# Kernel tuning notes

Measured on AMD Instinct MI355X. Metric: run time of the kernel, lower is better.

The kernel has to match this reference:

```python
import jax, jax.numpy as jnp
import numpy as np
from jax import lax


def _conv2d(x, w, b, pad):
    out = lax.conv_general_dilated(x, w, window_strides=(1, 1),
                                   padding=[(pad, pad), (pad, pad)])
    return out + b[None, :, None, None]


def _modulated_deform_conv(x, off_w, off_b, w, b, k, pad):
    """Modulated deformable conv (deformable_groups=1, stride=1, 'same' pad)."""
    B, C, H, W = x.shape
    K2 = k * k
    # offset/mask conv: 3*K2 channels -> (dy, dx, mask_logits)
    om = _conv2d(x, off_w, off_b, pad)              # [B, 3*K2, H, W]
    dy, dx, mlog = om[:, :K2], om[:, K2:2 * K2], om[:, 2 * K2:]
    mask = jax.nn.sigmoid(mlog)                     # [B, K2, H, W]

    xp = jnp.pad(x, ((0, 0), (0, 0), (pad, pad), (pad, pad)))
    Hp, Wp = H + 2 * pad, W + 2 * pad
    Ho, Wo = H, W                                   # stride 1, pad = k//2

    ky, kx = jnp.meshgrid(jnp.arange(k), jnp.arange(k), indexing='ij')
    ky = ky.reshape(1, K2, 1, 1).astype(x.dtype)
    kx = kx.reshape(1, K2, 1, 1).astype(x.dtype)
    iy = jnp.arange(Ho, dtype=x.dtype).reshape(1, 1, Ho, 1)
    ix = jnp.arange(Wo, dtype=x.dtype).reshape(1, 1, 1, Wo)

    py = iy + ky + dy                               # [B, K2, Ho, Wo] sample y (padded coords)
    px = ix + kx + dx                               # [B, K2, Ho, Wo] sample x

    y0f = jnp.floor(py); x0f = jnp.floor(px)
    ty = py - y0f; tx = px - x0f
    y0 = y0f.astype(jnp.int32); x0 = x0f.astype(jnp.int32)
    y1 = y0 + 1; x1 = x0 + 1

    xp_flat = xp.reshape(B, C, Hp * Wp)

    def gather(yi, xi):
        valid = ((yi >= 0) & (yi < Hp) & (xi >= 0) & (xi < Wp)).astype(x.dtype)
        yc = jnp.clip(yi, 0, Hp - 1)
        xc = jnp.clip(xi, 0, Wp - 1)
        idx = (yc * Wp + xc).reshape(B, 1, K2 * Ho * Wo)
        v = jnp.take_along_axis(xp_flat, idx, axis=2).reshape(B, C, K2, Ho, Wo)
        return v * valid[:, None]                   # zero-pad outside

    w00 = ((1 - ty) * (1 - tx))[:, None]
    w01 = ((1 - ty) * tx)[:, None]
    w10 = (ty * (1 - tx))[:, None]
    w11 = (ty * tx)[:, None]

    cols = (gather(y0, x0) * w00 + gather(y0, x1) * w01 +
            gather(y1, x0) * w10 + gather(y1, x1) * w11)
    cols = cols * mask[:, None]                     # [B, C, K2, Ho, Wo]

    O = w.shape[0]
    out = jnp.einsum('bckhw,ock->bohw', cols, w.reshape(O, C, K2))
    return out + b[None, :, None, None]


def setup_inputs() -> dict:
    key = jax.random.key(0)
    ks = jax.random.split(key, 12)
    B, Cin, H, W = 8, 64, 56, 56
    Ch = 128  # out_channels // 2

    def rn(k, shape, scale):
        return jax.random.normal(k, shape, dtype=jnp.float32) * scale

    return {
        'x': rn(ks[0], (B, Cin, H, W), 1.0),
        'w3': rn(ks[1], (Ch, Cin, 3, 3), 0.05),
        'b3': rn(ks[2], (Ch,), 0.05),
        'off3_w': rn(ks[3], (3 * 9, Cin, 3, 3), 0.01),
        'off3_b': rn(ks[4], (3 * 9,), 0.01),
        'w5': rn(ks[5], (Ch, Cin, 5, 5), 0.03),
        'b5': rn(ks[6], (Ch,), 0.05),
        'off5_w': rn(ks[7], (3 * 25, Cin, 5, 5), 0.01),
        'off5_b': rn(ks[8], (3 * 25,), 0.01),
        'sub_w': rn(ks[9], (Ch, Cin, 1, 1), 0.1),
        'sub_b': rn(ks[10], (Ch,), 0.05),
    }


def reference(x, w3, b3, off3_w, off3_b, w5, b5, off5_w, off5_b, sub_w, sub_b):
    x3 = _modulated_deform_conv(x, off3_w, off3_b, w3, b3, k=3, pad=1)
    x5 = _modulated_deform_conv(x, off5_w, off5_b, w5, b5, k=5, pad=2)
    xs = _conv2d(x, sub_w, sub_b, pad=0)            # 1x1 shortcut projection
    x3 = x3 + xs
    x5 = x5 + xs
    out = jnp.concatenate((x3, x5), axis=1)
    return jax.nn.relu(out)
```

## Files before the change

### kernel.cpp

```cpp
#include <hip/hip_runtime.h>
#include <math.h>

typedef __attribute__((ext_vector_type(8))) short short8;
typedef __attribute__((ext_vector_type(4))) float f32x4;

#define US_XP    0
#define N_XP     (8*60*60*64)
#define US_WOFF  (US_XP + N_XP)
#define N_WOFF   (25*2*8*64*8)
#define US_W5    (US_WOFF + N_WOFF)
#define N_W5     (26*2*8*64*8)
#define US_W3    (US_W5 + N_W5)
#define N_W3     (10*2*8*64*8)
#define US_TOT   (US_W3 + N_W3)
#define FB_BYTES (((US_TOT*2) + 15) & ~15)
#define F_BOM    0
#define F_B5     128
#define F_B3     256
#define F_OM     384
#define N_OM     (8*128*3136)

__device__ __forceinline__ unsigned short f2bf(float f) {
    union { float f; unsigned u; } v; v.f = f;
    unsigned r = v.u + 0x7FFFu + ((v.u >> 16) & 1u);
    return (unsigned short)(r >> 16);
}
__device__ __forceinline__ float bf2f(unsigned short u) {
    union { unsigned u; float f; } v; v.u = ((unsigned)u) << 16; return v.f;
}

__global__ __launch_bounds__(256) void prep_kernel(
    const float* __restrict__ x,
    const float* __restrict__ w3, const float* __restrict__ b3,
    const float* __restrict__ off3w, const float* __restrict__ off3b,
    const float* __restrict__ w5, const float* __restrict__ b5,
    const float* __restrict__ off5w, const float* __restrict__ off5b,
    const float* __restrict__ subw, const float* __restrict__ subb,
    unsigned short* __restrict__ us, float* __restrict__ fb)
{
    const int NTOT = US_TOT + 384;
    for (int i = blockIdx.x*256 + threadIdx.x; i < NTOT; i += gridDim.x*256) {
        if (i < US_TOT) {
            float v = 0.f;
            if (i < US_WOFF) {
                int c = i & 63, t = i >> 6;
                int xx = t % 60; t /= 60;
                int yy = t % 60; int b = t / 60;
                int y = yy - 2, xc = xx - 2;
                if ((unsigned)y < 56u && (unsigned)xc < 56u)
                    v = x[((b*64 + c)*56 + y)*56 + xc];
            } else {
                int j, mode;
                if (i < US_W5)      { j = i - US_WOFF; mode = 0; }
                else if (i < US_W3) { j = i - US_W5;   mode = 1; }
                else                { j = i - US_W3;   mode = 2; }
                int j8   = j & 7;
                int lane = (j >> 3) & 63;
                int oct  = (j >> 9) & 7;
                int kt   = (j >> 12) & 1;
                int tap  = j >> 13;
                int oc   = oct*16 + (lane & 15);
                int c    = kt*32 + (lane >> 4)*8 + j8;
                if (mode == 0) {
                    if (oc < 27) {
                        int ky = tap/5, kx = tap%5;
                        if (ky>=1 && ky<=3 && kx>=1 && kx<=3)
                            v = off3w[((oc*64 + c)*3 + (ky-1))*3 + (kx-1)];
                    } else if (oc < 102) {
                        v = off5w[((oc-27)*64 + c)*25 + tap];
                    }
                } else if (mode == 1) {
                    v = (tap < 25) ? w5[(oc*64 + c)*25 + tap] : subw[oc*64 + c];
                } else {
                    v = (tap < 9) ? w3[(oc*64 + c)*9 + tap] : subw[oc*64 + c];
                }
            }
            us[i] = f2bf(v);
        } else {
            int fj = i - US_TOT;
            float v;
            if (fj < 128)      v = (fj < 27) ? off3b[fj] : ((fj < 102) ? off5b[fj-27] : 0.f);
            else if (fj < 256) { int o = fj-128; v = b5[o] + subb[o]; }
            else               { int o = fj-256; v = b3[o] + subb[o]; }
            fb[fj] = v;
        }
    }
}

template<bool DEFORM>
__global__ __launch_bounds__(256, 3) void convm(
    const unsigned short* __restrict__ xp,
    const float* __restrict__ om,
    float* __restrict__ out,
    const unsigned short* __restrict__ wpA, const float* __restrict__ biasA,
    const unsigned short* __restrict__ wpB, const float* __restrict__ biasB,
    int ksA, int ksB, int ntA, int ntB, int omc0A, int omc0B,
    int outc0A, int outc0B, int out_cs)
{
    const int z = blockIdx.z;
    const unsigned short* wp = z ? wpB : wpA;
    const float* bias = z ? biasB : biasA;
    const int KS    = z ? ksB : ksA;
    const int ntaps = z ? ntB : ntA;
    const int omc0  = z ? omc0B : omc0A;
    const int outc0 = z ? outc0B : outc0A;
    const int K2 = KS*KS;
    const int PAD = (KS == 3) ? 1 : 2;
    const int SHIFT = 2 - PAD;
    const int HP = 56 + 2*PAD;

    const int b    = blockIdx.y;
    const int pix0 = blockIdx.x * 32;
    const int lane = threadIdx.x & 63;
    const int wave = threadIdx.x >> 6;
    const int r15  = lane & 15;
    const int q4   = lane >> 4;

    __shared__ unsigned short cols[2][32*72];

    f32x4 acc[2][2] = {{{0.f,0.f,0.f,0.f},{0.f,0.f,0.f,0.f}},
                       {{0.f,0.f,0.f,0.f},{0.f,0.f,0.f,0.f}}};

    const unsigned short* xpb = xp + (size_t)b * (60*60*64);

    auto stage = [&](int tap, unsigned short* buf) {
        const int cl = r15 * 4;
        int ky = 0, kx = 0;
        if (tap < K2) { ky = tap / KS; kx = tap - ky*KS; }
#pragma unroll
        for (int it = 0; it < 2; ++it) {
            const int px  = wave*8 + it*4 + q4;
            const int pix = pix0 + px;
            const int oy  = pix / 56;
            const int ox  = pix - oy*56;
            ushort4 val;
            if (DEFORM && tap < K2) {
                const float dy = om[(size_t)(b*128 + omc0 + tap)*3136 + pix];
                const float dx = om[(size_t)(b*128 + omc0 + K2 + tap)*3136 + pix];
                const float ml = om[(size_t)(b*128 + omc0 + 2*K2 + tap)*3136 + pix];
                const float mask = 1.f / (1.f + __expf(-ml));
                const float py = (float)(oy + ky) + dy;
                const float qx = (float)(ox + kx) + dx;
                const float y0f = floorf(py), x0f = floorf(qx);
                const float ty = py - y0f, tx = qx - x0f;
                const int y0 = (int)y0f, x0 = (int)x0f;
                const int y1 = y0 + 1,   x1 = x0 + 1;
                float w00 = (1.f-ty)*(1.f-tx)*mask;
                float w01 = (1.f-ty)*tx*mask;
                float w10 = ty*(1.f-tx)*mask;
                float w11 = ty*tx*mask;
                const bool vy0 = (y0>=0)&(y0<HP), vy1 = (y1>=0)&(y1<HP);
                const bool vx0 = (x0>=0)&(x0<HP), vx1 = (x1>=0)&(x1<HP);
                if (!(vy0&vx0)) w00 = 0.f;
                if (!(vy0&vx1)) w01 = 0.f;
                if (!(vy1&vx0)) w10 = 0.f;
                if (!(vy1&vx1)) w11 = 0.f;
                const int yc0 = min(max(y0,0),HP-1)+SHIFT;
                const int yc1 = min(max(y1,0),HP-1)+SHIFT;
                const int xc0 = min(max(x0,0),HP-1)+SHIFT;
                const int xc1 = min(max(x1,0),HP-1)+SHIFT;
                ushort4 u00 = *(const ushort4*)(xpb + (yc0*60+xc0)*64 + cl);
                ushort4 u01 = *(const ushort4*)(xpb + (yc0*60+xc1)*64 + cl);
                ushort4 u10 = *(const ushort4*)(xpb + (yc1*60+xc0)*64 + cl);
                ushort4 u11 = *(const ushort4*)(xpb + (yc1*60+xc1)*64 + cl);
                val.x = f2bf(bf2f(u00.x)*w00 + bf2f(u01.x)*w01 + bf2f(u10.x)*w10 + bf2f(u11.x)*w11);
                val.y = f2bf(bf2f(u00.y)*w00 + bf2f(u01.y)*w01 + bf2f(u10.y)*w10 + bf2f(u11.y)*w11);
                val.z = f2bf(bf2f(u00.z)*w00 + bf2f(u01.z)*w01 + bf2f(u10.z)*w10 + bf2f(u11.z)*w11);
                val.w = f2bf(bf2f(u00.w)*w00 + bf2f(u01.w)*w01 + bf2f(u10.w)*w10 + bf2f(u11.w)*w11);
            } else {
                int yy, xx;
                if (DEFORM) { yy = oy + 2; xx = ox + 2; }
                else        { yy = oy + ky + SHIFT; xx = ox + kx + SHIFT; }
                val = *(const ushort4*)(xpb + (yy*60+xx)*64 + cl);
            }
            *(ushort4*)&buf[px*72 + cl] = val;
        }
    };

    auto gemm = [&](int tap, const unsigned short* buf) {
#pragma unroll
        for (int kt = 0; kt < 2; ++kt) {
            const unsigned short* wt = wp + ((size_t)((tap*2 + kt)*8 + wave*2)*64 + lane)*8;
            short8 a0 = *(const short8*)wt;
            short8 a1 = *(const short8*)(wt + 64*8);
            const unsigned short* bp = buf + r15*72 + kt*32 + q4*8;
            short8 b0 = *(const short8*)bp;
            short8 b1 = *(const short8*)(bp + 16*72);
            acc[0][0] = __builtin_amdgcn_mfma_f32_16x16x32_bf16(a0, b0, acc[0][0], 0, 0, 0);
            acc[1][0] = __builtin_amdgcn_mfma_f32_16x16x32_bf16(a1, b0, acc[1][0], 0, 0, 0);
            acc[0][1] = __builtin_amdgcn_mfma_f32_16x16x32_bf16(a0, b1, acc[0][1], 0, 0, 0);
            acc[1][1] = __builtin_amdgcn_mfma_f32_16x16x32_bf16(a1, b1, acc[1][1], 0, 0, 0);
        }
    };

    stage(0, cols[0]);
    __syncthreads();
    for (int t = 0; t < ntaps; ++t) {
        if (t + 1 < ntaps) stage(t + 1, cols[(t+1) & 1]);
        gemm(t, cols[t & 1]);
        __syncthreads();
    }

#pragma unroll
    for (int j = 0; j < 2; ++j) {
#pragma unroll
        for (int pt = 0; pt < 2; ++pt) {
#pragma unroll
            for (int reg = 0; reg < 4; ++reg) {
                const int oc  = (wave*2 + j)*16 + q4*4 + reg;
                const int pix = pix0 + pt*16 + r15;
                float v = acc[j][pt][reg] + bias[oc];
                if (DEFORM) v = fmaxf(v, 0.f);
                out[((size_t)b*out_cs + outc0 + oc)*3136 + pix] = v;
            }
        }
    }
}

extern "C" void kernel_launch(void* const* d_in, const int* in_sizes, int n_in,
                              void* d_out, int out_size, void* d_ws, size_t ws_size,
                              hipStream_t stream)
{
    (void)in_sizes; (void)n_in; (void)out_size; (void)ws_size;
    const float* x     = (const float*)d_in[0];
    const float* w3    = (const float*)d_in[1];
    const float* b3    = (const float*)d_in[2];
    const float* off3w = (const float*)d_in[3];
    const float* off3b = (const float*)d_in[4];
    const float* w5    = (const float*)d_in[5];
    const float* b5    = (const float*)d_in[6];
    const float* off5w = (const float*)d_in[7];
    const float* off5b = (const float*)d_in[8];
    const float* subw  = (const float*)d_in[9];
    const float* subb  = (const float*)d_in[10];

    unsigned short* us = (unsigned short*)d_ws;
    float* fb  = (float*)((char*)d_ws + FB_BYTES);
    float* omb = fb + F_OM;
    float* out = (float*)d_out;

    prep_kernel<<<dim3(1024), dim3(256), 0, stream>>>(
        x, w3, b3, off3w, off3b, w5, b5, off5w, off5b, subw, subb, us, fb);

    convm<false><<<dim3(98, 8, 1), dim3(256), 0, stream>>>(
        us + US_XP, nullptr, omb,
        us + US_WOFF, fb + F_BOM, us + US_WOFF, fb + F_BOM,
        5, 5, 25, 25, 0, 0, 0, 0, 128);

    convm<true><<<dim3(98, 8, 2), dim3(256), 0, stream>>>(
        us + US_XP, omb, out,
        us + US_W5, fb + F_B5, us + US_W3, fb + F_B3,
        5, 3, 26, 10, 27, 0, 128, 0, 256);
}
```

Baseline: 187.0 us.

## Precompute deform sampling offsets/weights and widen gathers with larger pixel tiles

A new meta kernel precomputes, for every tap and pixel, the four bilinear corner byte offsets and bf16-packed mask-scaled weights, so the deformable conv no longer computes the sigmoid, floor and clamps inline. The staging loop now loads 16-byte channel chunks (8 lanes per pixel) rather than 8-byte ones. It blends with packed bf16 conversions. The deformable conv uses 64-pixel tiles, with the 3x3/5x5 branch interleaved on blockIdx.x instead of z. The trade-off is an extra launch plus writing and re-reading the offset/weight buffers, and bf16 rounding of the interpolation weights.

New measurement: 190.9 us. 2.1% more time.

```diff
diff --git a/kernel.cpp b/kernel.cpp
--- a/kernel.cpp
+++ b/kernel.cpp
@@ -1,4 +1,5 @@
 #include <hip/hip_runtime.h>
+#include <hip/hip_bf16.h>
 #include <math.h>
 
 typedef __attribute__((ext_vector_type(8))) short short8;
@@ -19,14 +20,26 @@
 #define F_B3     256
 #define F_OM     384
 #define N_OM     (8*128*3136)
+#define N_ITEMS  (8*34*3136)
+#define F_OFFS   (F_OM + N_OM)
+#define F_WTS    (F_OFFS + N_ITEMS*4)
 
 __device__ __forceinline__ unsigned short f2bf(float f) {
     union { float f; unsigned u; } v; v.f = f;
     unsigned r = v.u + 0x7FFFu + ((v.u >> 16) & 1u);
     return (unsigned short)(r >> 16);
 }
-__device__ __forceinline__ float bf2f(unsigned short u) {
-    union { unsigned u; float f; } v; v.u = ((unsigned)u) << 16; return v.f;
+__device__ __forceinline__ unsigned pack2(float lo, float hi) {
+    __hip_bfloat162 h = __float22bfloat162_rn(make_float2(lo, hi));
+    return *(unsigned*)&h;
+}
+__device__ __forceinline__ unsigned blend2(unsigned a, unsigned b, unsigned c, unsigned d,
+                                           float w00, float w01, float w10, float w11) {
+    float lo = __uint_as_float(a << 16) * w00 + __uint_as_float(b << 16) * w01
+             + __uint_as_float(c << 16) * w10 + __uint_as_float(d << 16) * w11;
+    float hi = __uint_as_float(a & 0xffff0000u) * w00 + __uint_as_float(b & 0xffff0000u) * w01
+             + __uint_as_float(c & 0xffff0000u) * w10 + __uint_as_float(d & 0xffff0000u) * w11;
+    return pack2(lo, hi);
 }
 
 __global__ __launch_bounds__(256) void prep_kernel(
@@ -87,109 +100,140 @@
     }
 }
 
-template<bool DEFORM>
+__global__ __launch_bounds__(256) void meta_kernel(
+    const float* __restrict__ om, int4* __restrict__ offs, uint2* __restrict__ wts)
+{
+    const int idx = blockIdx.x*256 + threadIdx.x;
+    const int pix = idx % 3136;
+    const int r   = idx / 3136;
+    const int t   = r % 34;
+    const int b   = r / 34;
+    int ky, kx, cdy, cdx, cml, HP, SH;
+    if (t < 25) { ky = t/5;  kx = t%5;  cdy = 27+t; cdx = 52+t; cml = 77+t; HP = 60; SH = 0; }
+    else { int tt = t-25; ky = tt/3; kx = tt%3; cdy = tt; cdx = 9+tt; cml = 18+tt; HP = 58; SH = 1; }
+    const int oy = pix/56, ox = pix - oy*56;
+    const size_t base = (size_t)b*128*3136 + pix;
+    const float dy = om[base + (size_t)cdy*3136];
+    const float dx = om[base + (size_t)cdx*3136];
+    const float ml = om[base + (size_t)cml*3136];
+    const float mask = 1.f / (1.f + __expf(-ml));
+    const float py = (float)(oy + ky) + dy;
+    const float qx = (float)(ox + kx) + dx;
+    const float y0f = floorf(py), x0f = floorf(qx);
+    const float ty = py - y0f, tx = qx - x0f;
+    const int y0 = (int)y0f, x0 = (int)x0f, y1 = y0+1, x1 = x0+1;
+    float w00 = (1.f-ty)*(1.f-tx)*mask;
+    float w01 = (1.f-ty)*tx*mask;
+    float w10 = ty*(1.f-tx)*mask;
+    float w11 = ty*tx*mask;
+    const bool vy0 = (unsigned)y0 < (unsigned)HP, vy1 = (unsigned)y1 < (unsigned)HP;
+    const bool vx0 = (unsigned)x0 < (unsigned)HP, vx1 = (unsigned)x1 < (unsigned)HP;
+    if (!(vy0 && vx0)) w00 = 0.f;
+    if (!(vy0 && vx1)) w01 = 0.f;
+    if (!(vy1 && vx0)) w10 = 0.f;
+    if (!(vy1 && vx1)) w11 = 0.f;
+    const int yc0 = min(max(y0,0),HP-1)+SH, yc1 = min(max(y1,0),HP-1)+SH;
+    const int xc0 = min(max(x0,0),HP-1)+SH, xc1 = min(max(x1,0),HP-1)+SH;
+    offs[idx] = make_int4((yc0*60+xc0)<<7, (yc0*60+xc1)<<7, (yc1*60+xc0)<<7, (yc1*60+xc1)<<7);
+    wts[idx]  = make_uint2(pack2(w00,w01), pack2(w10,w11));
+}
+
+template<int PXT, bool DEFORM>
 __global__ __launch_bounds__(256, 3) void convm(
     const unsigned short* __restrict__ xp,
-    const float* __restrict__ om,
+    const int4* __restrict__ offs, const uint2* __restrict__ wts,
     float* __restrict__ out,
     const unsigned short* __restrict__ wpA, const float* __restrict__ biasA,
     const unsigned short* __restrict__ wpB, const float* __restrict__ biasB,
-    int ksA, int ksB, int ntA, int ntB, int omc0A, int omc0B,
+    int ntA, int ntB, int k2A, int k2B, int tofsA, int tofsB,
     int outc0A, int outc0B, int out_cs)
 {
-    const int z = blockIdx.z;
-    const unsigned short* wp = z ? wpB : wpA;
-    const float* bias = z ? biasB : biasA;
-    const int KS    = z ? ksB : ksA;
-    const int ntaps = z ? ntB : ntA;
-    const int omc0  = z ? omc0B : omc0A;
-    const int outc0 = z ? outc0B : outc0A;
-    const int K2 = KS*KS;
-    const int PAD = (KS == 3) ? 1 : 2;
-    const int SHIFT = 2 - PAD;
-    const int HP = 56 + 2*PAD;
+    const int kind  = DEFORM ? (int)(blockIdx.x & 1) : 0;
+    const int pxblk = DEFORM ? (int)(blockIdx.x >> 1) : (int)blockIdx.x;
+    const unsigned short* wp = kind ? wpB : wpA;
+    const float* bias = kind ? biasB : biasA;
+    const int ntaps = kind ? ntB : ntA;
+    const int K2    = kind ? k2B : k2A;
+    const int tofs  = kind ? tofsB : tofsA;
+    const int outc0 = kind ? outc0B : outc0A;
 
     const int b    = blockIdx.y;
-    const int pix0 = blockIdx.x * 32;
+    const int pix0 = pxblk * PXT;
     const int lane = threadIdx.x & 63;
     const int wave = threadIdx.x >> 6;
-    const int r15  = lane & 15;
-    const int q4   = lane >> 4;
-
-    __shared__ unsigned short cols[2][32*72];
-
-    f32x4 acc[2][2] = {{{0.f,0.f,0.f,0.f},{0.f,0.f,0.f,0.f}},
-                       {{0.f,0.f,0.f,0.f},{0.f,0.f,0.f,0.f}}};
-
-    const unsigned short* xpb = xp + (size_t)b * (60*60*64);
+    const int r15 = lane & 15, q4 = lane >> 4;
+    const int cg  = lane & 7,  pr = lane >> 3;
+
+    constexpr int NIT = PXT / 32;
+    constexpr int NPT = PXT / 16;
+
+    __shared__ unsigned short cols[2][PXT*72];
+
+    f32x4 acc[2][NPT];
+#pragma unroll
+    for (int i = 0; i < 2; ++i)
+#pragma unroll
+        for (int pt = 0; pt < NPT; ++pt) acc[i][pt] = (f32x4){0.f,0.f,0.f,0.f};
+
+    const unsigned short* xpb = xp + (size_t)b*(60*60*64);
+    const char* xb = (const char*)xpb;
+
+    int coff[NIT], mbase[NIT];
+#pragma unroll
+    for (int it = 0; it < NIT; ++it) {
+        const int px  = wave*(NIT*8) + it*8 + pr;
+        const int pix = pix0 + px;
+        const int oy  = pix/56, ox = pix - oy*56;
+        coff[it]  = (((oy+2)*60) + ox + 2) << 7;
+        mbase[it] = (b*34 + tofs)*3136 + pix;
+    }
 
     auto stage = [&](int tap, unsigned short* buf) {
-        const int cl = r15 * 4;
-        int ky = 0, kx = 0;
-        if (tap < K2) { ky = tap / KS; kx = tap - ky*KS; }
-#pragma unroll
-        for (int it = 0; it < 2; ++it) {
-            const int px  = wave*8 + it*4 + q4;
-            const int pix = pix0 + px;
-            const int oy  = pix / 56;
-            const int ox  = pix - oy*56;
-            ushort4 val;
-            if (DEFORM && tap < K2) {
-                const float dy = om[(size_t)(b*128 + omc0 + tap)*3136 + pix];
-                const float dx = om[(size_t)(b*128 + omc0 + K2 + tap)*3136 + pix];
-                const float ml = om[(size_t)(b*128 + omc0 + 2*K2 + tap)*3136 + pix];
-                const float mask = 1.f / (1.f + __expf(-ml));
-                const float py = (float)(oy + ky) + dy;
-                const float qx = (float)(ox + kx) + dx;
-                const float y0f = floorf(py), x0f = floorf(qx);
-                const float ty = py - y0f, tx = qx - x0f;
-                const int y0 = (int)y0f, x0 = (int)x0f;
-                const int y1 = y0 + 1,   x1 = x0 + 1;
-                float w00 = (1.f-ty)*(1.f-tx)*mask;
-                float w01 = (1.f-ty)*tx*mask;
-                float w10 = ty*(1.f-tx)*mask;
-                float w11 = ty*tx*mask;
-                const bool vy0 = (y0>=0)&(y0<HP), vy1 = (y1>=0)&(y1<HP);
-                const bool vx0 = (x0>=0)&(x0<HP), vx1 = (x1>=0)&(x1<HP);
-                if (!(vy0&vx0)) w00 = 0.f;
-                if (!(vy0&vx1)) w01 = 0.f;
-                if (!(vy1&vx0)) w10 = 0.f;
-                if (!(vy1&vx1)) w11 = 0.f;
-                const int yc0 = min(max(y0,0),HP-1)+SHIFT;
-                const int yc1 = min(max(y1,0),HP-1)+SHIFT;
-                const int xc0 = min(max(x0,0),HP-1)+SHIFT;
-                const int xc1 = min(max(x1,0),HP-1)+SHIFT;
-                ushort4 u00 = *(const ushort4*)(xpb + (yc0*60+xc0)*64 + cl);
-                ushort4 u01 = *(const ushort4*)(xpb + (yc0*60+xc1)*64 + cl);
-                ushort4 u10 = *(const ushort4*)(xpb + (yc1*60+xc0)*64 + cl);
-                ushort4 u11 = *(const ushort4*)(xpb + (yc1*60+xc1)*64 + cl);
-                val.x = f2bf(bf2f(u00.x)*w00 + bf2f(u01.x)*w01 + bf2f(u10.x)*w10 + bf2f(u11.x)*w11);
-                val.y = f2bf(bf2f(u00.y)*w00 + bf2f(u01.y)*w01 + bf2f(u10.y)*w10 + bf2f(u11.y)*w11);
-                val.z = f2bf(bf2f(u00.z)*w00 + bf2f(u01.z)*w01 + bf2f(u10.z)*w10 + bf2f(u11.z)*w11);
-                val.w = f2bf(bf2f(u00.w)*w00 + bf2f(u01.w)*w01 + bf2f(u10.w)*w10 + bf2f(u11.w)*w11);
+        int koff = 0;
+        if (!DEFORM) { int ky = tap/5, kx = tap - ky*5; koff = ((ky-2)*60 + (kx-2)) << 7; }
+#pragma unroll
+        for (int it = 0; it < NIT; ++it) {
+            const int px = wave*(NIT*8) + it*8 + pr;
+            uint4 res;
+            if (!DEFORM) {
+                res = *(const uint4*)(xb + coff[it] + koff + cg*16);
+            } else if (tap >= K2) {
+                res = *(const uint4*)(xb + coff[it] + cg*16);
             } else {
-                int yy, xx;
-                if (DEFORM) { yy = oy + 2; xx = ox + 2; }
-                else        { yy = oy + ky + SHIFT; xx = ox + kx + SHIFT; }
-                val = *(const ushort4*)(xpb + (yy*60+xx)*64 + cl);
+                const int mi = mbase[it] + tap*3136;
+                const int4 o4 = offs[mi];
+                const uint2 wq = wts[mi];
+                const float w00 = __uint_as_float(wq.x << 16);
+                const float w01 = __uint_as_float(wq.x & 0xffff0000u);
+                const float w10 = __uint_as_float(wq.y << 16);
+                const float w11 = __uint_as_float(wq.y & 0xffff0000u);
+                const uint4 qa = *(const uint4*)(xb + o4.x + cg*16);
+                const uint4 qb = *(const uint4*)(xb + o4.y + cg*16);
+                const uint4 qc = *(const uint4*)(xb + o4.z + cg*16);
+                const uint4 qd = *(const uint4*)(xb + o4.w + cg*16);
+                res.x = blend2(qa.x, qb.x, qc.x, qd.x, w00, w01, w10, w11);
+                res.y = blend2(qa.y, qb.y, qc.y, qd.y, w00, w01, w10, w11);
+                res.z = blend2(qa.z, qb.z, qc.z, qd.z, w00, w01, w10, w11);
+                res.w = blend2(qa.w, qb.w, qc.w, qd.w, w00, w01, w10, w11);
             }
-            *(ushort4*)&buf[px*72 + cl] = val;
+            *(uint4*)&buf[px*72 + cg*8] = res;
         }
     };
 
     auto gemm = [&](int tap, const unsigned short* buf) {
 #pragma unroll
         for (int kt = 0; kt < 2; ++kt) {
-            const unsigned short* wt = wp + ((size_t)((tap*2 + kt)*8 + wave*2)*64 + lane)*8;
-            short8 a0 = *(const short8*)wt;
-            short8 a1 = *(const short8*)(wt + 64*8);
-            const unsigned short* bp = buf + r15*72 + kt*32 + q4*8;
-            short8 b0 = *(const short8*)bp;
-            short8 b1 = *(const short8*)(bp + 16*72);
-            acc[0][0] = __builtin_amdgcn_mfma_f32_16x16x32_bf16(a0, b0, acc[0][0], 0, 0, 0);
-            acc[1][0] = __builtin_amdgcn_mfma_f32_16x16x32_bf16(a1, b0, acc[1][0], 0, 0, 0);
-            acc[0][1] = __builtin_amdgcn_mfma_f32_16x16x32_bf16(a0, b1, acc[0][1], 0, 0, 0);
-            acc[1][1] = __builtin_amdgcn_mfma_f32_16x16x32_bf16(a1, b1, acc[1][1], 0, 0, 0);
+            short8 Af[2];
+#pragma unroll
+            for (int i = 0; i < 2; ++i)
+                Af[i] = *(const short8*)(wp + ((size_t)((tap*2+kt)*8 + wave*2 + i)*64 + lane)*8);
+#pragma unroll
+            for (int pt = 0; pt < NPT; ++pt) {
+                short8 Bf = *(const short8*)(buf + (pt*16 + r15)*72 + kt*32 + q4*8);
+#pragma unroll
+                for (int i = 0; i < 2; ++i)
+                    acc[i][pt] = __builtin_amdgcn_mfma_f32_16x16x32_bf16(Af[i], Bf, acc[i][pt], 0, 0, 0);
+            }
         }
     };
 
@@ -202,18 +246,16 @@
     }
 
 #pragma unroll
-    for (int j = 0; j < 2; ++j) {
-#pragma unroll
-        for (int pt = 0; pt < 2; ++pt) {
-#pragma unroll
-            for (int reg = 0; reg < 4; ++reg) {
-                const int oc  = (wave*2 + j)*16 + q4*4 + reg;
-                const int pix = pix0 + pt*16 + r15;
-                float v = acc[j][pt][reg] + bias[oc];
-                if (DEFORM) v = fmaxf(v, 0.f);
-                out[((size_t)b*out_cs + outc0 + oc)*3136 + pix] = v;
-            }
-        }
+    for (int i = 0; i < 2; ++i)
+#pragma unroll
+    for (int pt = 0; pt < NPT; ++pt)
+#pragma unroll
+    for (int reg = 0; reg < 4; ++reg) {
+        const int oc  = (wave*2 + i)*16 + q4*4 + reg;
+        const int pix = pix0 + pt*16 + r15;
+        float v = acc[i][pt][reg] + bias[oc];
+        if (DEFORM) v = fmaxf(v, 0.f);
+        out[((size_t)b*out_cs + outc0 + oc)*3136 + pix] = v;
     }
 }
 
@@ -235,20 +277,24 @@
     const float* subb  = (const float*)d_in[10];
 
     unsigned short* us = (unsigned short*)d_ws;
-    float* fb  = (float*)((char*)d_ws + FB_BYTES);
-    float* omb = fb + F_OM;
-    float* out = (float*)d_out;
+    float* fb   = (float*)((char*)d_ws + FB_BYTES);
+    float* omb  = fb + F_OM;
+    int4*  offs = (int4*)(fb + F_OFFS);
+    uint2* wts  = (uint2*)(fb + F_WTS);
+    float* out  = (float*)d_out;
 
     prep_kernel<<<dim3(1024), dim3(256), 0, stream>>>(
         x, w3, b3, off3w, off3b, w5, b5, off5w, off5b, subw, subb, us, fb);
 
-    convm<false><<<dim3(98, 8, 1), dim3(256), 0, stream>>>(
-        us + US_XP, nullptr, omb,
+    convm<32, false><<<dim3(98, 8), dim3(256), 0, stream>>>(
+        us + US_XP, nullptr, nullptr, omb,
         us + US_WOFF, fb + F_BOM, us + US_WOFF, fb + F_BOM,
-        5, 5, 25, 25, 0, 0, 0, 0, 128);
-
-    convm<true><<<dim3(98, 8, 2), dim3(256), 0, stream>>>(
-        us + US_XP, omb, out,
+        25, 25, 25, 25, 0, 0, 0, 0, 128);
+
+    meta_kernel<<<dim3(N_ITEMS/256), dim3(256), 0, stream>>>(omb, offs, wts);
+
+    convm<64, true><<<dim3(98, 8), dim3(256), 0, stream>>>(
+        us + US_XP, offs, wts, out,
         us + US_W5, fb + F_B5, us + US_W3, fb + F_B3,
-        5, 3, 26, 10, 27, 0, 128, 0, 256);
-}
+        26, 10, 25, 9, 0, 25, 128, 0, 256);
+}
```
